# Optimization experiments

Measured on AMD Instinct MI355X. Metric: run time of the kernel, lower is better.

## Reference

```python
import jax, jax.numpy as jnp
import numpy as np
from jax import lax

# norse LIFParameters defaults
DT = 0.001
TAU_SYN_INV = 200.0   # 1 / 5e-3
TAU_MEM_INV = 100.0   # 1 / 1e-2
V_TH = 1.0
ALPHA = 100.0
SEQ_LENGTH = 32

# Heaviside forward with SuperSpike surrogate gradient (method='super')
@jax.custom_vjp
def spike_super(x):
    return (x > 0).astype(x.dtype)
def _ss_fwd(x):
    return (x > 0).astype(x.dtype), x
def _ss_bwd(x, g):
    return (g / (ALPHA * jnp.abs(x) + 1.0) ** 2,)
spike_super.defvjp(_ss_fwd, _ss_bwd)

# Heaviside forward with tanh surrogate gradient (method='tanh')
@jax.custom_vjp
def spike_tanh(x):
    return (x > 0).astype(x.dtype)
def _st_fwd(x):
    return (x > 0).astype(x.dtype), x
def _st_bwd(x, g):
    t = jnp.tanh(ALPHA * x)
    return (g * (1.0 - t * t),)
spike_tanh.defvjp(_st_fwd, _st_bwd)

def conv2d(x, w, b):
    # stride 1, padding 1, dilation 1, groups 1 (padding == padding_h == k//2 here)
    y = lax.conv_general_dilated(x, w, (1, 1), [(1, 1), (1, 1)],
                                 dimension_numbers=('NCHW', 'OIHW', 'NCHW'))
    return y + b[None, :, None, None]

def lif_step(inp, v, i, spike_fn):
    # norse lif_feed_forward_step
    v_dec = v + DT * TAU_MEM_INV * (-v + i)
    i_dec = i - DT * TAU_SYN_INV * i
    z = spike_fn(v_dec - V_TH)
    v_new = (1.0 - z) * v_dec  # v_reset = 0
    return z, v_new, i_dec + inp

def setup_inputs():
    key = jax.random.key(0)
    ks = jax.random.split(key, 9)
    B, Cin, Cout, H, W, K = 8, 64, 64, 32, 32, 3
    stdv = 1.0 / float(np.sqrt(4 * Cin * K * K))
    u = lambda k, shape: jax.random.uniform(k, shape, jnp.float32, -stdv, stdv)
    return {
        'input': jax.random.normal(ks[0], (B, Cin, H, W), jnp.float32),
        'h0': jax.random.normal(ks[1], (B, Cout, H, W), jnp.float32),
        'c0': jax.random.normal(ks[2], (B, Cout, H, W), jnp.float32),
        'weight_ih': u(ks[3], (4 * Cout, Cin, K, K)),
        'weight_hh': u(ks[4], (4 * Cout, Cout, K, K)),
        'weight_ch': u(ks[5], (3 * Cout, Cout, K, K)),
        'bias_ih': u(ks[6], (4 * Cout,)),
        'bias_hh': u(ks[7], (4 * Cout,)),
        'bias_ch': u(ks[8], (3 * Cout,)),
    }

def reference(input, h0, c0, weight_ih, weight_hh, weight_ch, bias_ih, bias_hh, bias_ch):
    C = weight_hh.shape[0] // 4
    wh = conv2d(h0, weight_hh, bias_hh)   # [B,4C,H,W]
    wc = conv2d(c0, weight_ch, bias_ch)   # [B,3C,H,W]
    # peephole: i,f gates get wc[:, :2C], g gate gets zeros (wc_blank), o gate gets wc[:, 2C:]
    whc = wh + jnp.concatenate([wc[:, :2 * C], jnp.zeros_like(wc[:, :C]), wc[:, 2 * C:]], axis=1)
    z0 = jnp.zeros_like(wh[:, :C])        # [B,C,H,W]
    neg_inf = jnp.full_like(z0, -jnp.inf)
    v_enc0 = jnp.zeros_like(input)

    def step(carry, t):
        v_enc, vi, ii, vf, fi, vg, gi, mi, mf, mg, mo = carry
        # constant-current LIF encoder step
        v = v_enc + DT * TAU_MEM_INV * (-v_enc + input)
        x = spike_super(v - V_TH)
        v_enc = v - x * v  # reset to 0 on spike
        wx = conv2d(x, weight_ih, bias_ih)
        wxhc = wx + whc
        _, vi, ii = lif_step(wxhc[:, :C], vi, ii, spike_super)
        _, vf, fi = lif_step(wxhc[:, C:2 * C], vf, fi, spike_super)
        _, vg, gi = lif_step(wxhc[:, 2 * C:3 * C], vg, gi, spike_tanh)
        # NOTE: original code passes sg (the just-updated g state) into the o-gate step
        _, vo, _ = lif_step(wxhc[:, 3 * C:], vg, gi, spike_super)
        upd = t >= 1  # stack(v[1:]).max(0): skip first timestep
        mi = jnp.where(upd, jnp.maximum(mi, vi), mi)
        mf = jnp.where(upd, jnp.maximum(mf, vf), mf)
        mg = jnp.where(upd, jnp.maximum(mg, vg), mg)
        mo = jnp.where(upd, jnp.maximum(mo, vo), mo)
        return (v_enc, vi, ii, vf, fi, vg, gi, mi, mf, mg, mo), None

    carry0 = (v_enc0, z0, z0, z0, z0, z0, z0, neg_inf, neg_inf, neg_inf, neg_inf)
    carry, _ = lax.scan(step, carry0, jnp.arange(SEQ_LENGTH))
    mi, mf, mg, mo = carry[7], carry[8], carry[9], carry[10]
    c1 = mf * c0 + mi * mg
    h1 = mo * jnp.tanh(c1)
    return (h1, c1)
```

## Files before the change

### kernel.cpp

```cpp
#include <hip/hip_runtime.h>
#include <hip/hip_bf16.h>
#include <hip/hip_fp16.h>

typedef unsigned short u16;
typedef signed char s8;
typedef __attribute__((ext_vector_type(8))) short short8;
typedef __attribute__((ext_vector_type(4))) float f32x4;
typedef __attribute__((ext_vector_type(4))) int i32x4;

#define NELEM 524288
#define PADW 34
#define PLANE 73984
#define SEQ 32

__device__ inline void split3(float v, u16& a, u16& b, u16& c) {
  __hip_bfloat16 h1 = __float2bfloat16(v);
  float r1 = v - __bfloat162float(h1);
  __hip_bfloat16 h2 = __float2bfloat16(r1);
  float r2 = r1 - __bfloat162float(h2);
  __hip_bfloat16 h3 = __float2bfloat16(r2);
  a = *reinterpret_cast<u16*>(&h1);
  b = *reinterpret_cast<u16*>(&h2);
  c = *reinterpret_cast<u16*>(&h3);
}

__device__ inline void gload16(const void* g, void* l) {
  typedef const __attribute__((address_space(1))) void* gp_t;
  typedef __attribute__((address_space(3))) void* lp_t;
  __builtin_amdgcn_global_load_lds((gp_t)g, (lp_t)l, 16, 0, 0);
}

__global__ void encode_kernel(const float* __restrict__ input, s8* __restrict__ xp) {
  int e = blockIdx.x * 256 + threadIdx.x;
  int c = e & 63;
  int pp = (e >> 6) % 1156;
  int b = e / (1156 * 64);
  int py = pp / 34, px = pp - py * 34;
  size_t base = (size_t)b * PLANE + (size_t)pp * 64 + c;
  bool interior = (py >= 1 && py <= 32 && px >= 1 && px <= 32);
  const double DMI = 0.001 * 100.0;
  double inp = interior ? (double)input[(size_t)(((b << 6) + c) << 10) + (py - 1) * 32 + (px - 1)] : 0.0;
  double ve = 0.0;
  for (int t = 0; t < SEQ; ++t) {
    double v = ve + DMI * (inp - ve);
    bool x = interior && (v > 1.0);
    ve = x ? 0.0 : v;
    xp[(size_t)t * (8 * PLANE) + base] = x ? (s8)1 : (s8)0;
  }
}

__global__ void prep_hc_kernel(const float* __restrict__ h0, const float* __restrict__ c0,
                               u16* __restrict__ h1, u16* __restrict__ h2, u16* __restrict__ h3,
                               u16* __restrict__ c1, u16* __restrict__ c2, u16* __restrict__ c3) {
  int e = blockIdx.x * 256 + threadIdx.x;
  int c = e & 63;
  int pp = (e >> 6) % 1156;
  int b = e / (1156 * 64);
  int py = pp / 34, px = pp - py * 34;
  size_t dst = (size_t)b * PLANE + (size_t)pp * 64 + c;
  bool interior = (py >= 1 && py <= 32 && px >= 1 && px <= 32);
  u16 a = 0, bb = 0, cc = 0, d = 0, ee = 0, ff = 0;
  if (interior) {
    size_t src = (size_t)(((b << 6) + c) << 10) + (py - 1) * 32 + (px - 1);
    split3(h0[src], a, bb, cc);
    split3(c0[src], d, ee, ff);
  }
  h1[dst] = a; h2[dst] = bb; h3[dst] = cc;
  c1[dst] = d; c2[dst] = ee; c3[dst] = ff;
}

__global__ void prep_w_kernel(const float* __restrict__ wih, const float* __restrict__ whh,
                              const float* __restrict__ wch,
                              s8* __restrict__ iq0, s8* __restrict__ iq1, s8* __restrict__ iq2,
                              u16* __restrict__ hh1, u16* __restrict__ hh2, u16* __restrict__ hh3,
                              u16* __restrict__ ch1, u16* __restrict__ ch2, u16* __restrict__ ch3) {
  int t = blockIdx.x * 256 + threadIdx.x;
  int c = t & 63;
  int row = (t >> 6) & 511;
  int tap = t >> 15;
  if (row < 192) {
    float v = wih[(size_t)((row << 6) + c) * 9 + tap];
    int Wi = (int)llrint((double)v * 268435456.0);
    int b0 = (Wi << 24) >> 24;
    int W1 = (Wi - b0) >> 8;
    int b1 = (W1 << 24) >> 24;
    int b2 = (W1 - b1) >> 8;
    size_t d = (size_t)(tap * 192 + row) * 64 + c;
    iq0[d] = (s8)b0; iq1[d] = (s8)b1; iq2[d] = (s8)b2;
  } else {
    const float* src; u16 *d1, *d2, *d3; int m, Mtot;
    if (row < 384) { src = whh; m = row - 192; Mtot = 192; d1 = hh1; d2 = hh2; d3 = hh3; }
    else           { src = wch; m = row - 384; Mtot = 128; d1 = ch1; d2 = ch2; d3 = ch3; }
    float v = src[(size_t)((m << 6) + c) * 9 + tap];
    u16 a, b, cc; split3(v, a, b, cc);
    size_t d = (size_t)(tap * Mtot + m) * 64 + c;
    d1[d] = a; d2[d] = b; d3[d] = cc;
  }
}

__global__ __launch_bounds__(256, 2) void conv0_kernel(
    const s8* __restrict__ X, const s8* __restrict__ W0p, const s8* __restrict__ W1p,
    const s8* __restrict__ W2p, float* __restrict__ out) {
  __shared__ uint4 ldsx4[816];
  __shared__ uint4 ldsw4[1536];
  char* ldsx = (char*)ldsx4;
  char* ldsw = (char*)ldsw4;

  const int tid = threadIdx.x;
  const int lane = tid & 63;
  const int wid = tid >> 6;
  const int mtile = blockIdx.x;
  const int rg = blockIdx.y;
  const int img = blockIdx.z;

  {
    const char* src = (const char*)X + (size_t)img * PLANE + (size_t)rg * 4 * (PADW * 64);
    for (int q = tid; q < 816; q += 256) {
      int L = q << 4;
      gload16(src + (L ^ (((L >> 7) & 3) << 4)), ldsx + L);
    }
  }

  const s8* wps[3] = {W0p, W1p, W2p};
  const size_t wbase = (size_t)mtile * 64 * 64;
  auto stageW = [&](int tap, int buf) {
#pragma unroll
    for (int part = 0; part < 3; ++part) {
      const char* gsrc = (const char*)(wps[part] + (size_t)tap * 192 * 64 + wbase);
      int L = tid << 4;
      gload16(gsrc + (L ^ (((L >> 7) & 3) << 4)), ldsw + buf * 12288 + part * 4096 + L);
    }
  };
  stageW(0, 0);
  __syncthreads();

  i32x4 acc[3][2][4];
#pragma unroll
  for (int p = 0; p < 3; ++p)
#pragma unroll
    for (int i = 0; i < 2; ++i)
#pragma unroll
      for (int j = 0; j < 4; ++j)
#pragma unroll
        for (int k = 0; k < 4; ++k) acc[p][i][j][k] = 0;

  const int wm = wid >> 1, wn = wid & 1;
  const int kg = lane >> 4;

  for (int tap = 0; tap < 9; ++tap) {
    if (tap < 8) stageW(tap + 1, (tap + 1) & 1);
    char* wb = ldsw + (tap & 1) * 12288;
    const int kh = tap / 3, kw = tap - kh * 3;
    i32x4 bfr[4];
#pragma unroll
    for (int fn = 0; fn < 4; ++fn) {
      int p = wn * 64 + fn * 16 + (lane & 15);
      int r = p >> 5, w = p & 31;
      int pL = (r + kh) * PADW + (w + kw);
      int byte = (pL * 64 + kg * 16) ^ (((pL >> 1) & 3) << 4);
      bfr[fn] = *reinterpret_cast<const i32x4*>(ldsx + byte);
    }
#pragma unroll
    for (int part = 0; part < 3; ++part) {
      i32x4 af[2];
#pragma unroll
      for (int fm = 0; fm < 2; ++fm) {
        int m = wm * 32 + fm * 16 + (lane & 15);
        int byte = (m * 64 + kg * 16) ^ (((m >> 1) & 3) << 4);
        af[fm] = *reinterpret_cast<const i32x4*>(wb + part * 4096 + byte);
      }
      __builtin_amdgcn_s_setprio(1);
#pragma unroll
      for (int fm = 0; fm < 2; ++fm)
#pragma unroll
        for (int fn = 0; fn < 4; ++fn)
          acc[part][fm][fn] = __builtin_amdgcn_mfma_i32_16x16x64_i8(af[fm], bfr[fn], acc[part][fm][fn], 0, 0, 0);
      __builtin_amdgcn_s_setprio(0);
    }
    __syncthreads();
  }

  size_t obase = (size_t)img * (192 * 1024);
  const double S0 = 1.0 / 268435456.0;
#pragma unroll
  for (int fm = 0; fm < 2; ++fm)
#pragma unroll
    for (int fn = 0; fn < 4; ++fn) {
      int pcol = rg * 128 + wn * 64 + fn * 16 + (lane & 15);
      int mrow0 = mtile * 64 + wm * 32 + fm * 16 + (lane >> 4) * 4;
#pragma unroll
      for (int r2 = 0; r2 < 4; ++r2) {
        long long tot = ((long long)acc[2][fm][fn][r2] << 16) +
                        (long long)(acc[1][fm][fn][r2] * 256 + acc[0][fm][fn][r2]);
        out[obase + (size_t)(mrow0 + r2) * 1024 + pcol] = (float)((double)tot * S0);
      }
    }
}

__global__ __launch_bounds__(256) void conv1_kernel(
    const u16* __restrict__ Ah0, const u16* __restrict__ Ah1, const u16* __restrict__ Ah2,
    const u16* __restrict__ Ac0, const u16* __restrict__ Ac1, const u16* __restrict__ Ac2,
    const u16* __restrict__ Wh0, const u16* __restrict__ Wh1, const u16* __restrict__ Wh2,
    const u16* __restrict__ Wc0, const u16* __restrict__ Wc1, const u16* __restrict__ Wc2,
    float* __restrict__ outh, float* __restrict__ outc) {
  __shared__ uint4 ldsx4[3 * 1088];
  __shared__ uint4 ldsw4[3 * 512];
  char* ldsx = (char*)ldsx4;
  char* ldsw = (char*)ldsw4;

  const int tid = threadIdx.x;
  const int lane = tid & 63;
  const int wid = tid >> 6;
  const bool isC = blockIdx.x >= 3;
  const int mtile = isC ? blockIdx.x - 3 : blockIdx.x;
  const int Mtot = isC ? 128 : 192;
  const int rg = blockIdx.y;
  const int img = blockIdx.z;
  const u16* aps[3] = {isC ? Ac0 : Ah0, isC ? Ac1 : Ah1, isC ? Ac2 : Ah2};
  const u16* wps[3] = {isC ? Wc0 : Wh0, isC ? Wc1 : Wh1, isC ? Wc2 : Wh2};
  float* out = isC ? outc : outh;

  {
    size_t abase = (size_t)img * PLANE + (size_t)rg * 2 * (PADW * 64);
#pragma unroll
    for (int pl = 0; pl < 3; ++pl) {
      const char* src = (const char*)(aps[pl] + abase);
      for (int q = tid; q < 1088; q += 256) {
        int L = q << 4;
        gload16(src + (L ^ (((L >> 7) & 7) << 4)), ldsx + pl * 17408 + L);
      }
    }
  }

  const size_t wrowbase = (size_t)mtile * 64 * 64;
  auto stageW = [&](int tap) {
#pragma unroll
    for (int part = 0; part < 3; ++part) {
      const char* gsrc = (const char*)(wps[part] + (size_t)tap * Mtot * 64 + wrowbase);
#pragma unroll
      for (int half = 0; half < 2; ++half) {
        int L = half * 4096 + tid * 16;
        gload16(gsrc + (L ^ (((L >> 7) & 7) << 4)), ldsw + part * 8192 + L);
      }
    }
  };

  f32x4 acc[2][2];
#pragma unroll
  for (int i = 0; i < 2; ++i)
#pragma unroll
    for (int j = 0; j < 2; ++j)
#pragma unroll
      for (int k = 0; k < 4; ++k) acc[i][j][k] = 0.f;

  const int wm = wid >> 1, wn = wid & 1;

  for (int tap = 0; tap < 9; ++tap) {
    if (tap) __syncthreads();
    stageW(tap);
    __syncthreads();
    const int kh = tap / 3, kw = tap - kh * 3;
#pragma unroll
    for (int khalf = 0; khalf < 2; ++khalf) {
      short8 af[3][2];
#pragma unroll
      for (int part = 0; part < 3; ++part)
#pragma unroll
        for (int fm = 0; fm < 2; ++fm) {
          int m = wm * 32 + fm * 16 + (lane & 15);
          int byte = (m * 128 + khalf * 64 + (lane >> 4) * 16) ^ ((m & 7) << 4);
          af[part][fm] = *reinterpret_cast<const short8*>(ldsw + part * 8192 + byte);
        }
#pragma unroll
      for (int pl = 0; pl < 3; ++pl) {
        short8 bfr[2];
#pragma unroll
        for (int fn = 0; fn < 2; ++fn) {
          int p = wn * 32 + fn * 16 + (lane & 15);
          int r = p >> 5, w = p & 31;
          int pL = (r + kh) * PADW + (w + kw);
          int byte = (pL * 128 + khalf * 64 + (lane >> 4) * 16) ^ ((pL & 7) << 4);
          bfr[fn] = *reinterpret_cast<const short8*>(ldsx + pl * 17408 + byte);
        }
        constexpr int npt[3] = {3, 2, 1};
        __builtin_amdgcn_s_setprio(1);
#pragma unroll
        for (int part = 0; part < 3; ++part) {
          if (part < npt[pl]) {
#pragma unroll
            for (int fm = 0; fm < 2; ++fm)
#pragma unroll
              for (int fn = 0; fn < 2; ++fn)
                acc[fm][fn] = __builtin_amdgcn_mfma_f32_16x16x32_bf16(af[part][fm], bfr[fn], acc[fm][fn], 0, 0, 0);
          }
        }
        __builtin_amdgcn_s_setprio(0);
      }
    }
  }

  size_t obase = (size_t)img * Mtot * 1024;
#pragma unroll
  for (int fm = 0; fm < 2; ++fm)
#pragma unroll
    for (int fn = 0; fn < 2; ++fn) {
      int pcol = rg * 64 + wn * 32 + fn * 16 + (lane & 15);
      int mrow0 = mtile * 64 + wm * 32 + fm * 16 + (lane >> 4) * 4;
#pragma unroll
      for (int r2 = 0; r2 < 4; ++r2)
        out[obase + (size_t)(mrow0 + r2) * 1024 + pcol] = acc[fm][fn][r2];
    }
}

__global__ void scan_kernel(const float* __restrict__ wx,
                            const float* __restrict__ wh,
                            const float* __restrict__ wcb,
                            const float* __restrict__ bih, const float* __restrict__ bhh,
                            const float* __restrict__ bch,
                            double* __restrict__ st, const float* __restrict__ c0,
                            float* __restrict__ outp, int t0, int nt) {
  const double DMI = 0.001 * 100.0;
  const double DSI = 0.001 * 200.0;
  int e = blockIdx.x * 256 + threadIdx.x;
  int hw = e & 1023;
  int c = (e >> 10) & 63;
  int b = e >> 16;
  size_t o0 = ((size_t)b * 192 + c) * 1024 + hw;
  size_t w0 = ((size_t)b * 128 + c) * 1024 + hw;
  double cI = ((double)wh[o0] + (double)bhh[c]) + ((double)wcb[w0] + (double)bch[c]);
  double cF = ((double)wh[o0 + 64 * 1024] + (double)bhh[64 + c]) +
              ((double)wcb[w0 + 64 * 1024] + (double)bch[64 + c]);
  double cG = (double)wh[o0 + 128 * 1024] + (double)bhh[128 + c];
  double bI = (double)bih[c], bF = (double)bih[64 + c], bG = (double)bih[128 + c];

  double vi, ii, vf, fi, vg, gi, mi, mf, mg, mo;
  if (t0 == 0) {
    vi = ii = vf = fi = vg = gi = 0.0;
    mi = mf = mg = mo = -INFINITY;
  } else {
    vi = st[0 * NELEM + e]; ii = st[1 * NELEM + e];
    vf = st[2 * NELEM + e]; fi = st[3 * NELEM + e];
    vg = st[4 * NELEM + e]; gi = st[5 * NELEM + e];
    mi = st[6 * NELEM + e]; mf = st[7 * NELEM + e];
    mg = st[8 * NELEM + e]; mo = st[9 * NELEM + e];
  }
  for (int t = 0; t < nt; ++t) {
    const float* wp = wx + (size_t)(t * 8 + b) * (192 * 1024);
    double inpI = ((double)wp[(size_t)c * 1024 + hw] + bI) + cI;
    double inpF = ((double)wp[(size_t)(64 + c) * 1024 + hw] + bF) + cF;
    double inpG = ((double)wp[(size_t)(128 + c) * 1024 + hw] + bG) + cG;
    double vd = vi + DMI * (ii - vi);
    vi = (vd > 1.0) ? 0.0 : vd;
    ii = (ii - DSI * ii) + inpI;
    vd = vf + DMI * (fi - vf);
    vf = (vd > 1.0) ? 0.0 : vd;
    fi = (fi - DSI * fi) + inpF;
    vd = vg + DMI * (gi - vg);
    vg = (vd > 1.0) ? 0.0 : vd;
    gi = (gi - DSI * gi) + inpG;
    double vod = vg + DMI * (gi - vg);
    double vo = (vod > 1.0) ? 0.0 : vod;
    if (t0 + t >= 1) {
      mi = fmax(mi, vi); mf = fmax(mf, vf);
      mg = fmax(mg, vg); mo = fmax(mo, vo);
    }
  }
  if (t0 + nt >= SEQ) {
    double c1 = mf * (double)c0[e] + mi * mg;
    outp[e] = (float)(mo * tanh(c1));
    outp[NELEM + e] = (float)c1;
  } else {
    st[0 * NELEM + e] = vi; st[1 * NELEM + e] = ii;
    st[2 * NELEM + e] = vf; st[3 * NELEM + e] = fi;
    st[4 * NELEM + e] = vg; st[5 * NELEM + e] = gi;
    st[6 * NELEM + e] = mi; st[7 * NELEM + e] = mf;
    st[8 * NELEM + e] = mg; st[9 * NELEM + e] = mo;
  }
}

extern "C" void kernel_launch(void* const* d_in, const int* in_sizes, int n_in,
                              void* d_out, int out_size, void* d_ws, size_t ws_size,
                              hipStream_t stream) {
  const float* input = (const float*)d_in[0];
  const float* h0    = (const float*)d_in[1];
  const float* c0    = (const float*)d_in[2];
  const float* wih   = (const float*)d_in[3];
  const float* whh   = (const float*)d_in[4];
  const float* wch   = (const float*)d_in[5];
  const float* bih   = (const float*)d_in[6];
  const float* bhh   = (const float*)d_in[7];
  const float* bch   = (const float*)d_in[8];
  char* ws = (char*)d_ws;

  size_t off = 0;
  auto take = [&](size_t bytes) { size_t o = off; off += (bytes + 255) & ~(size_t)255; return o; };
  size_t oXp  = take((size_t)SEQ * 8 * PLANE);
  size_t oH1  = take((size_t)8 * PLANE * 2);
  size_t oH2  = take((size_t)8 * PLANE * 2);
  size_t oH3  = take((size_t)8 * PLANE * 2);
  size_t oC1  = take((size_t)8 * PLANE * 2);
  size_t oC2  = take((size_t)8 * PLANE * 2);
  size_t oC3  = take((size_t)8 * PLANE * 2);
  size_t oIq0 = take((size_t)9 * 192 * 64);
  size_t oIq1 = take((size_t)9 * 192 * 64);
  size_t oIq2 = take((size_t)9 * 192 * 64);
  size_t oHh1 = take((size_t)9 * 192 * 64 * 2);
  size_t oHh2 = take((size_t)9 * 192 * 64 * 2);
  size_t oHh3 = take((size_t)9 * 192 * 64 * 2);
  size_t oCh1 = take((size_t)9 * 128 * 64 * 2);
  size_t oCh2 = take((size_t)9 * 128 * 64 * 2);
  size_t oCh3 = take((size_t)9 * 128 * 64 * 2);
  size_t oWh  = take((size_t)8 * 192 * 1024 * 4);
  size_t oWc  = take((size_t)8 * 128 * 1024 * 4);
  size_t fixedEnd = off;

  const size_t chunkBytes = (size_t)8 * 192 * 1024 * 4;
  int chunk;
  size_t oWx, oSt;
  if (fixedEnd + 32 * chunkBytes <= ws_size) {
    chunk = 32;
    oWx = fixedEnd;
    oSt = fixedEnd;
  } else {
    oSt = take((size_t)10 * NELEM * 8);
    size_t fe2 = off;
    chunk = 16;
    while (chunk > 1 && fe2 + (size_t)chunk * chunkBytes > ws_size) chunk >>= 1;
    oWx = fe2;
  }

  s8* xp   = (s8*)(ws + oXp);
  u16* h1p = (u16*)(ws + oH1); u16* h2p = (u16*)(ws + oH2); u16* h3p = (u16*)(ws + oH3);
  u16* c1p = (u16*)(ws + oC1); u16* c2p = (u16*)(ws + oC2); u16* c3p = (u16*)(ws + oC3);
  s8* iq0  = (s8*)(ws + oIq0); s8* iq1 = (s8*)(ws + oIq1); s8* iq2 = (s8*)(ws + oIq2);
  u16* hh1 = (u16*)(ws + oHh1); u16* hh2 = (u16*)(ws + oHh2); u16* hh3 = (u16*)(ws + oHh3);
  u16* ch1 = (u16*)(ws + oCh1); u16* ch2 = (u16*)(ws + oCh2); u16* ch3 = (u16*)(ws + oCh3);
  float* whb = (float*)(ws + oWh);
  float* wcb = (float*)(ws + oWc);
  double* st = (double*)(ws + oSt);
  float* wxb = (float*)(ws + oWx);

  encode_kernel<<<2312, 256, 0, stream>>>(input, xp);
  prep_hc_kernel<<<2312, 256, 0, stream>>>(h0, c0, h1p, h2p, h3p, c1p, c2p, c3p);
  prep_w_kernel<<<1152, 256, 0, stream>>>(wih, whh, wch, iq0, iq1, iq2,
                                          hh1, hh2, hh3, ch1, ch2, ch3);

  conv1_kernel<<<dim3(5, 16, 8), 256, 0, stream>>>(
      h1p, h2p, h3p, c1p, c2p, c3p,
      hh1, hh2, hh3, ch1, ch2, ch3, whb, wcb);

  for (int t0 = 0; t0 < SEQ; t0 += chunk) {
    conv0_kernel<<<dim3(3, 8, 8 * chunk), 256, 0, stream>>>(
        xp + (size_t)t0 * 8 * PLANE, iq0, iq1, iq2, wxb);
    scan_kernel<<<2048, 256, 0, stream>>>(wxb, whb, wcb, bih, bhh, bch,
                                          st, c0, (float*)d_out, t0, chunk);
  }
}
```

Measured before the change: 235.0 us.

## Fuse per-timestep input conv with LIF gate scan in one persistent kernel

Replaces the separate conv0 + scan kernels, which wrote the full 32-step wx tensor to global memory, with a fused kernel where each block owns one gate slice and pixel tile and loops over all timesteps. It does the int8 MFMA conv for two timesteps at a time, then updates the LIF state in registers, keeping only running maxima. Input planes are prefetched into a 4-slot LDS ring and weights are double-buffered per tap. A small final kernel combines the gate maxima into h1/c1. This removes a large global round trip, but grid parallelism drops (768 blocks running a long serial loop) and weights are restaged for every timestep.

```diff
diff --git a/kernel.cpp b/kernel.cpp
--- a/kernel.cpp
+++ b/kernel.cpp
@@ -98,102 +98,174 @@
   }
 }
 
-__global__ __launch_bounds__(256, 2) void conv0_kernel(
+__global__ __launch_bounds__(256, 2) void fused_kernel(
     const s8* __restrict__ X, const s8* __restrict__ W0p, const s8* __restrict__ W1p,
-    const s8* __restrict__ W2p, float* __restrict__ out) {
-  __shared__ uint4 ldsx4[816];
-  __shared__ uint4 ldsw4[1536];
+    const s8* __restrict__ W2p,
+    const float* __restrict__ whb, const float* __restrict__ wcb,
+    const float* __restrict__ bih, const float* __restrict__ bhh,
+    const float* __restrict__ bch, float* __restrict__ maxbuf) {
+  __shared__ uint4 ldsx4[4 * 544];
+  __shared__ uint4 ldsw4[2 * 384];
   char* ldsx = (char*)ldsx4;
   char* ldsw = (char*)ldsw4;
+
+  const double DMI = 0.001 * 100.0;
+  const double DSI = 0.001 * 200.0;
+  const double S0 = 1.0 / 268435456.0;
 
   const int tid = threadIdx.x;
   const int lane = tid & 63;
   const int wid = tid >> 6;
-  const int mtile = blockIdx.x;
+  const int bx = blockIdx.x;
+  const int gate = bx >> 1, mh = bx & 1;
   const int rg = blockIdx.y;
-  const int img = blockIdx.z;
-
-  {
-    const char* src = (const char*)X + (size_t)img * PLANE + (size_t)rg * 4 * (PADW * 64);
-    for (int q = tid; q < 816; q += 256) {
-      int L = q << 4;
-      gload16(src + (L ^ (((L >> 7) & 3) << 4)), ldsx + L);
-    }
-  }
-
-  const s8* wps[3] = {W0p, W1p, W2p};
-  const size_t wbase = (size_t)mtile * 64 * 64;
-  auto stageW = [&](int tap, int buf) {
-#pragma unroll
-    for (int part = 0; part < 3; ++part) {
-      const char* gsrc = (const char*)(wps[part] + (size_t)tap * 192 * 64 + wbase);
-      int L = tid << 4;
-      gload16(gsrc + (L ^ (((L >> 7) & 3) << 4)), ldsw + buf * 12288 + part * 4096 + L);
-    }
-  };
-  stageW(0, 0);
-  __syncthreads();
-
-  i32x4 acc[3][2][4];
-#pragma unroll
-  for (int p = 0; p < 3; ++p)
-#pragma unroll
-    for (int i = 0; i < 2; ++i)
-#pragma unroll
-      for (int j = 0; j < 4; ++j)
-#pragma unroll
-        for (int k = 0; k < 4; ++k) acc[p][i][j][k] = 0;
-
+  const int b = blockIdx.z;
   const int wm = wid >> 1, wn = wid & 1;
   const int kg = lane >> 4;
 
-  for (int tap = 0; tap < 9; ++tap) {
-    if (tap < 8) stageW(tap + 1, (tap + 1) & 1);
-    char* wb = ldsw + (tap & 1) * 12288;
-    const int kh = tap / 3, kw = tap - kh * 3;
-    i32x4 bfr[4];
-#pragma unroll
-    for (int fn = 0; fn < 4; ++fn) {
-      int p = wn * 64 + fn * 16 + (lane & 15);
-      int r = p >> 5, w = p & 31;
-      int pL = (r + kh) * PADW + (w + kw);
-      int byte = (pL * 64 + kg * 16) ^ (((pL >> 1) & 3) << 4);
-      bfr[fn] = *reinterpret_cast<const i32x4*>(ldsx + byte);
-    }
-#pragma unroll
-    for (int part = 0; part < 3; ++part) {
-      i32x4 af[2];
-#pragma unroll
-      for (int fm = 0; fm < 2; ++fm) {
-        int m = wm * 32 + fm * 16 + (lane & 15);
+  const s8* wps[3] = {W0p, W1p, W2p};
+  const int wrow0 = gate * 64 + mh * 32;
+
+  auto xsrc = [&](int t) {
+    return (const char*)X + (size_t)(t * 8 + b) * PLANE + (size_t)rg * 2 * (PADW * 64);
+  };
+  auto stageW = [&](int tap, int buf) {
+    {
+      int part = tid >> 7;
+      int Lb = (tid & 127) << 4;
+      const char* g = (const char*)wps[part] + ((size_t)tap * 192 + wrow0) * 64
+                      + (Lb ^ (((Lb >> 7) & 3) << 4));
+      gload16(g, ldsw + buf * 6144 + part * 2048 + Lb);
+    }
+    if (tid < 128) {
+      int Lb = tid << 4;
+      const char* g = (const char*)wps[2] + ((size_t)tap * 192 + wrow0) * 64
+                      + (Lb ^ (((Lb >> 7) & 3) << 4));
+      gload16(g, ldsw + buf * 6144 + 2 * 2048 + Lb);
+    }
+  };
+  auto stageX = [&](int t) {
+    const char* src = xsrc(t);
+    char* dst = ldsx + (t & 3) * 8704;
+    for (int q = tid; q < 544; q += 256) {
+      int L = q << 4;
+      gload16(src + (L ^ (((L >> 7) & 3) << 4)), dst + L);
+    }
+  };
+
+  const int cbase = mh * 32 + wm * 16 + (lane >> 4) * 4;
+  const int hwbase = rg * 64 + wn * 32 + (lane & 15);
+  double cterm[8], v[8], cur[8];
+  float mx[8], mo[8];
+#pragma unroll
+  for (int fn = 0; fn < 2; ++fn)
+#pragma unroll
+    for (int r = 0; r < 4; ++r) {
+      int el = fn * 4 + r;
+      int row = gate * 64 + cbase + r;
+      int hw = hwbase + fn * 16;
+      double cI = (double)whb[((size_t)b * 192 + row) * 1024 + hw] + (double)bhh[row];
+      if (gate < 2)
+        cI = cI + ((double)wcb[((size_t)b * 128 + row) * 1024 + hw] + (double)bch[row]);
+      cterm[el] = (double)bih[row] + cI;
+      v[el] = 0.0; cur[el] = 0.0; mx[el] = -INFINITY; mo[el] = -INFINITY;
+    }
+
+  i32x4 acc[2][3][2];
+#pragma unroll
+  for (int t2 = 0; t2 < 2; ++t2)
+#pragma unroll
+    for (int p = 0; p < 3; ++p)
+#pragma unroll
+      for (int fn = 0; fn < 2; ++fn)
+#pragma unroll
+        for (int k = 0; k < 4; ++k) acc[t2][p][fn][k] = 0;
+
+  stageX(0); stageX(1); stageW(0, 0);
+  __syncthreads();
+  int wbuf = 0;
+
+  for (int tc = 0; tc < 16; ++tc) {
+#pragma unroll
+    for (int tap = 0; tap < 9; ++tap) {
+      if (!(tc == 15 && tap == 8)) stageW(tap == 8 ? 0 : tap + 1, wbuf ^ 1);
+      if (tc < 15 && tap < 8 && tid < 136) {
+        int gq = tap * 136 + tid;
+        int pl = gq >= 544;
+        int tn = 2 * tc + 2 + pl;
+        int L = (gq - pl * 544) << 4;
+        gload16(xsrc(tn) + (L ^ (((L >> 7) & 3) << 4)), ldsx + (tn & 3) * 8704 + L);
+      }
+      const int kh = tap / 3, kw = tap - (tap / 3) * 3;
+      char* wb = ldsw + wbuf * 6144;
+      i32x4 af[3];
+#pragma unroll
+      for (int p = 0; p < 3; ++p) {
+        int m = wm * 16 + (lane & 15);
         int byte = (m * 64 + kg * 16) ^ (((m >> 1) & 3) << 4);
-        af[fm] = *reinterpret_cast<const i32x4*>(wb + part * 4096 + byte);
-      }
-      __builtin_amdgcn_s_setprio(1);
-#pragma unroll
-      for (int fm = 0; fm < 2; ++fm)
-#pragma unroll
-        for (int fn = 0; fn < 4; ++fn)
-          acc[part][fm][fn] = __builtin_amdgcn_mfma_i32_16x16x64_i8(af[fm], bfr[fn], acc[part][fm][fn], 0, 0, 0);
-      __builtin_amdgcn_s_setprio(0);
-    }
-    __syncthreads();
-  }
-
-  size_t obase = (size_t)img * (192 * 1024);
-  const double S0 = 1.0 / 268435456.0;
-#pragma unroll
-  for (int fm = 0; fm < 2; ++fm)
-#pragma unroll
-    for (int fn = 0; fn < 4; ++fn) {
-      int pcol = rg * 128 + wn * 64 + fn * 16 + (lane & 15);
-      int mrow0 = mtile * 64 + wm * 32 + fm * 16 + (lane >> 4) * 4;
-#pragma unroll
-      for (int r2 = 0; r2 < 4; ++r2) {
-        long long tot = ((long long)acc[2][fm][fn][r2] << 16) +
-                        (long long)(acc[1][fm][fn][r2] * 256 + acc[0][fm][fn][r2]);
-        out[obase + (size_t)(mrow0 + r2) * 1024 + pcol] = (float)((double)tot * S0);
-      }
+        af[p] = *reinterpret_cast<const i32x4*>(wb + p * 2048 + byte);
+      }
+#pragma unroll
+      for (int t2 = 0; t2 < 2; ++t2) {
+        const char* xpl = ldsx + ((2 * tc + t2) & 3) * 8704;
+        i32x4 bfr[2];
+#pragma unroll
+        for (int fn = 0; fn < 2; ++fn) {
+          int p = wn * 32 + fn * 16 + (lane & 15);
+          int pL = ((p >> 5) + kh) * PADW + (p & 31) + kw;
+          int byte = (pL * 64 + kg * 16) ^ (((pL >> 1) & 3) << 4);
+          bfr[fn] = *reinterpret_cast<const i32x4*>(xpl + byte);
+        }
+        __builtin_amdgcn_s_setprio(1);
+#pragma unroll
+        for (int p = 0; p < 3; ++p)
+#pragma unroll
+          for (int fn = 0; fn < 2; ++fn)
+            acc[t2][p][fn] = __builtin_amdgcn_mfma_i32_16x16x64_i8(af[p], bfr[fn], acc[t2][p][fn], 0, 0, 0);
+        __builtin_amdgcn_s_setprio(0);
+      }
+      __syncthreads();
+      wbuf ^= 1;
+    }
+#pragma unroll
+    for (int t2 = 0; t2 < 2; ++t2) {
+      int t = 2 * tc + t2;
+#pragma unroll
+      for (int fn = 0; fn < 2; ++fn)
+#pragma unroll
+        for (int r = 0; r < 4; ++r) {
+          int el = fn * 4 + r;
+          int a0 = acc[t2][0][fn][r], a1 = acc[t2][1][fn][r], a2 = acc[t2][2][fn][r];
+          double wx = ((double)a2 * 65536.0 + (double)(a1 * 256 + a0)) * S0;
+          double inp = wx + cterm[el];
+          double vd = v[el] + DMI * (cur[el] - v[el]);
+          double vnew = (vd > 1.0) ? 0.0 : vd;
+          v[el] = vnew;
+          cur[el] = (cur[el] - DSI * cur[el]) + inp;
+          if (gate == 2) {
+            double vod = vnew + DMI * (cur[el] - vnew);
+            double vo = (vod > 1.0) ? 0.0 : vod;
+            if (t >= 1) mo[el] = fmaxf(mo[el], (float)vo);
+          }
+          if (t >= 1) mx[el] = fmaxf(mx[el], (float)vnew);
+        }
+#pragma unroll
+      for (int p = 0; p < 3; ++p)
+#pragma unroll
+        for (int fn = 0; fn < 2; ++fn)
+#pragma unroll
+          for (int k = 0; k < 4; ++k) acc[t2][p][fn][k] = 0;
+    }
+  }
+
+#pragma unroll
+  for (int fn = 0; fn < 2; ++fn)
+#pragma unroll
+    for (int r = 0; r < 4; ++r) {
+      int el = fn * 4 + r;
+      size_t e = ((size_t)b * 64 + cbase + r) * 1024 + hwbase + fn * 16;
+      maxbuf[(size_t)gate * NELEM + e] = mx[el];
+      if (gate == 2) maxbuf[(size_t)3 * NELEM + e] = mo[el];
     }
 }
 
@@ -312,70 +384,16 @@
     }
 }
 
-__global__ void scan_kernel(const float* __restrict__ wx,
-                            const float* __restrict__ wh,
-                            const float* __restrict__ wcb,
-                            const float* __restrict__ bih, const float* __restrict__ bhh,
-                            const float* __restrict__ bch,
-                            double* __restrict__ st, const float* __restrict__ c0,
-                            float* __restrict__ outp, int t0, int nt) {
-  const double DMI = 0.001 * 100.0;
-  const double DSI = 0.001 * 200.0;
+__global__ void final_kernel(const float* __restrict__ maxbuf, const float* __restrict__ c0,
+                             float* __restrict__ out) {
   int e = blockIdx.x * 256 + threadIdx.x;
-  int hw = e & 1023;
-  int c = (e >> 10) & 63;
-  int b = e >> 16;
-  size_t o0 = ((size_t)b * 192 + c) * 1024 + hw;
-  size_t w0 = ((size_t)b * 128 + c) * 1024 + hw;
-  double cI = ((double)wh[o0] + (double)bhh[c]) + ((double)wcb[w0] + (double)bch[c]);
-  double cF = ((double)wh[o0 + 64 * 1024] + (double)bhh[64 + c]) +
-              ((double)wcb[w0 + 64 * 1024] + (double)bch[64 + c]);
-  double cG = (double)wh[o0 + 128 * 1024] + (double)bhh[128 + c];
-  double bI = (double)bih[c], bF = (double)bih[64 + c], bG = (double)bih[128 + c];
-
-  double vi, ii, vf, fi, vg, gi, mi, mf, mg, mo;
-  if (t0 == 0) {
-    vi = ii = vf = fi = vg = gi = 0.0;
-    mi = mf = mg = mo = -INFINITY;
-  } else {
-    vi = st[0 * NELEM + e]; ii = st[1 * NELEM + e];
-    vf = st[2 * NELEM + e]; fi = st[3 * NELEM + e];
-    vg = st[4 * NELEM + e]; gi = st[5 * NELEM + e];
-    mi = st[6 * NELEM + e]; mf = st[7 * NELEM + e];
-    mg = st[8 * NELEM + e]; mo = st[9 * NELEM + e];
-  }
-  for (int t = 0; t < nt; ++t) {
-    const float* wp = wx + (size_t)(t * 8 + b) * (192 * 1024);
-    double inpI = ((double)wp[(size_t)c * 1024 + hw] + bI) + cI;
-    double inpF = ((double)wp[(size_t)(64 + c) * 1024 + hw] + bF) + cF;
-    double inpG = ((double)wp[(size_t)(128 + c) * 1024 + hw] + bG) + cG;
-    double vd = vi + DMI * (ii - vi);
-    vi = (vd > 1.0) ? 0.0 : vd;
-    ii = (ii - DSI * ii) + inpI;
-    vd = vf + DMI * (fi - vf);
-    vf = (vd > 1.0) ? 0.0 : vd;
-    fi = (fi - DSI * fi) + inpF;
-    vd = vg + DMI * (gi - vg);
-    vg = (vd > 1.0) ? 0.0 : vd;
-    gi = (gi - DSI * gi) + inpG;
-    double vod = vg + DMI * (gi - vg);
-    double vo = (vod > 1.0) ? 0.0 : vod;
-    if (t0 + t >= 1) {
-      mi = fmax(mi, vi); mf = fmax(mf, vf);
-      mg = fmax(mg, vg); mo = fmax(mo, vo);
-    }
-  }
-  if (t0 + nt >= SEQ) {
-    double c1 = mf * (double)c0[e] + mi * mg;
-    outp[e] = (float)(mo * tanh(c1));
-    outp[NELEM + e] = (float)c1;
-  } else {
-    st[0 * NELEM + e] = vi; st[1 * NELEM + e] = ii;
-    st[2 * NELEM + e] = vf; st[3 * NELEM + e] = fi;
-    st[4 * NELEM + e] = vg; st[5 * NELEM + e] = gi;
-    st[6 * NELEM + e] = mi; st[7 * NELEM + e] = mf;
-    st[8 * NELEM + e] = mg; st[9 * NELEM + e] = mo;
-  }
+  double mi = (double)maxbuf[e];
+  double mf = (double)maxbuf[NELEM + e];
+  double mg = (double)maxbuf[2 * (size_t)NELEM + e];
+  double mo = (double)maxbuf[3 * (size_t)NELEM + e];
+  double c1 = mf * (double)c0[e] + mi * mg;
+  out[e] = (float)(mo * tanh(c1));
+  out[NELEM + e] = (float)c1;
 }
 
 extern "C" void kernel_launch(void* const* d_in, const int* in_sizes, int n_in,
@@ -412,22 +430,7 @@
   size_t oCh3 = take((size_t)9 * 128 * 64 * 2);
   size_t oWh  = take((size_t)8 * 192 * 1024 * 4);
   size_t oWc  = take((size_t)8 * 128 * 1024 * 4);
-  size_t fixedEnd = off;
-
-  const size_t chunkBytes = (size_t)8 * 192 * 1024 * 4;
-  int chunk;
-  size_t oWx, oSt;
-  if (fixedEnd + 32 * chunkBytes <= ws_size) {
-    chunk = 32;
-    oWx = fixedEnd;
-    oSt = fixedEnd;
-  } else {
-    oSt = take((size_t)10 * NELEM * 8);
-    size_t fe2 = off;
-    chunk = 16;
-    while (chunk > 1 && fe2 + (size_t)chunk * chunkBytes > ws_size) chunk >>= 1;
-    oWx = fe2;
-  }
+  size_t oMx  = take((size_t)4 * NELEM * 4);
 
   s8* xp   = (s8*)(ws + oXp);
   u16* h1p = (u16*)(ws + oH1); u16* h2p = (u16*)(ws + oH2); u16* h3p = (u16*)(ws + oH3);
@@ -437,8 +440,7 @@
   u16* ch1 = (u16*)(ws + oCh1); u16* ch2 = (u16*)(ws + oCh2); u16* ch3 = (u16*)(ws + oCh3);
   float* whb = (float*)(ws + oWh);
   float* wcb = (float*)(ws + oWc);
-  double* st = (double*)(ws + oSt);
-  float* wxb = (float*)(ws + oWx);
+  float* mxb = (float*)(ws + oMx);
 
   encode_kernel<<<2312, 256, 0, stream>>>(input, xp);
   prep_hc_kernel<<<2312, 256, 0, stream>>>(h0, c0, h1p, h2p, h3p, c1p, c2p, c3p);
@@ -449,10 +451,8 @@
       h1p, h2p, h3p, c1p, c2p, c3p,
       hh1, hh2, hh3, ch1, ch2, ch3, whb, wcb);
 
-  for (int t0 = 0; t0 < SEQ; t0 += chunk) {
-    conv0_kernel<<<dim3(3, 8, 8 * chunk), 256, 0, stream>>>(
-        xp + (size_t)t0 * 8 * PLANE, iq0, iq1, iq2, wxb);
-    scan_kernel<<<2048, 256, 0, stream>>>(wxb, whb, wcb, bih, bhh, bch,
-                                          st, c0, (float*)d_out, t0, chunk);
-  }
-}
+  fused_kernel<<<dim3(6, 16, 8), 256, 0, stream>>>(
+      xp, iq0, iq1, iq2, whb, wcb, bih, bhh, bch, mxb);
+
+  final_kernel<<<2048, 256, 0, stream>>>(mxb, c0, (float*)d_out);
+}
```

New measurement: 285.6 us. 1.22x slower.
